# Performance work log

Hardware: AMD Instinct MI355X
Metric: run time of the kernel (lower is better)

## Reference

```python
import jax, jax.numpy as jnp
import numpy as np

B, S, H, K = 4, 2048, 1024, 4
DT, TAU_MIN, TAU_MAX = 0.1, 1.0, 5.0
SCALE = 0.01
LN_EPS = 1e-5


def setup_inputs() -> dict:
    key = jax.random.key(0)
    ks = jax.random.split(key, 8)
    inv = 1.0 / np.sqrt(H)
    return {
        "hidden_states": jax.random.normal(ks[0], (B, S, H), dtype=jnp.float32),
        "conv_w": jax.random.normal(ks[1], (H, K), dtype=jnp.float32) * 0.25,  # depthwise causal conv weights
        "W_rec": jax.random.normal(ks[2], (H, H), dtype=jnp.float32) * inv,    # Linear(H,H,bias=False).weight
        "tau_w1": jax.random.normal(ks[3], (2 * H, H // 2), dtype=jnp.float32) * (1.0 / np.sqrt(2 * H)),
        "tau_b1": jnp.zeros((H // 2,), dtype=jnp.float32),
        "tau_w2": jax.random.normal(ks[4], (H // 2, 1), dtype=jnp.float32) * (1.0 / np.sqrt(H // 2)),
        "tau_b2": jnp.zeros((1,), dtype=jnp.float32),
        "ln_g": jnp.ones((H,), dtype=jnp.float32),
        "ln_b": jnp.zeros((H,), dtype=jnp.float32),
    }


def _shortconv(x, conv_w):
    # depthwise causal conv over seq: x [B,S,H], conv_w [H,K]
    xp = jnp.pad(x, ((0, 0), (K - 1, 0), (0, 0)))
    out = jnp.zeros_like(x)
    for k in range(K):  # K=4, static small loop
        out = out + conv_w[None, None, :, k] * xp[:, k:k + x.shape[1], :]
    return out


def _liquid(x, W_rec, tau_w1, tau_b1, tau_w2, tau_b2, ln_g, ln_b):
    # x: [B,S,H] -> per-step gated recurrence with LayerNorm, via lax.scan
    def step(h, x_t):
        combined = jnp.concatenate([x_t, h], axis=-1)                  # [B,2H]
        tau_raw = jax.nn.sigmoid(
            jnp.tanh(combined @ tau_w1 + tau_b1) @ tau_w2 + tau_b2)    # [B,1]
        tau = TAU_MIN + (TAU_MAX - TAU_MIN) * tau_raw
        f_xh = jnp.tanh(x_t + h @ W_rec.T)                             # [B,H]
        h = h + DT * (-h + f_xh) / tau
        mu = jnp.mean(h, axis=-1, keepdims=True)
        var = jnp.mean((h - mu) ** 2, axis=-1, keepdims=True)
        h = (h - mu) / jnp.sqrt(var + LN_EPS) * ln_g + ln_b            # LayerNorm
        return h, h

    h0 = jnp.zeros((x.shape[0], H), dtype=x.dtype)
    _, liq = jax.lax.scan(step, h0, jnp.swapaxes(x, 0, 1))             # liq [S,B,H]
    return jnp.swapaxes(liq, 0, 1)


def reference(hidden_states, conv_w, W_rec, tau_w1, tau_b1, tau_w2, tau_b2, ln_g, ln_b):
    sc = _shortconv(hidden_states, conv_w)
    liq = _liquid(hidden_states, W_rec, tau_w1, tau_b1, tau_w2, tau_b2, ln_g, ln_b)
    return sc + SCALE * (liq - sc)
```

## Files before the change

### kernel.cpp

```cpp
#include <hip/hip_runtime.h>
#include <math.h>

#define BB   4
#define SS   2048
#define HH   1024
#define HHF  512
#define NWG  192
#define REC_WGS 128
#define NTH  256

__device__ __forceinline__ float dot4f(float4 a, float4 b){
  return a.x*b.x + a.y*b.y + a.z*b.z + a.w*b.w;
}

__device__ __forceinline__ float2 aload2(const float* p){
  unsigned long long v = __hip_atomic_load((const unsigned long long*)p,
                                           __ATOMIC_RELAXED, __HIP_MEMORY_SCOPE_AGENT);
  union { unsigned long long u; float2 f; } c; c.u = v; return c.f;
}
__device__ __forceinline__ void astore1(float* p, float v){
  __hip_atomic_store(p, v, __ATOMIC_RELAXED, __HIP_MEMORY_SCOPE_AGENT);
}
__device__ __forceinline__ float aload1(const float* p){
  return __hip_atomic_load(p, __ATOMIC_RELAXED, __HIP_MEMORY_SCOPE_AGENT);
}

__global__ __launch_bounds__(256) void transpose_w1h(const float* __restrict__ tw1,
                                                     float* __restrict__ w1hT){
  __shared__ float ts[32][33];
  int c  = threadIdx.x & 31;
  int r4 = (threadIdx.x >> 5) * 4;
  int bi = blockIdx.x * 32;
  int bm = blockIdx.y * 32;
  #pragma unroll
  for (int rr = 0; rr < 4; ++rr)
    ts[r4+rr][c] = tw1[(size_t)(1024 + bi + r4 + rr) * 512 + bm + c];
  __syncthreads();
  #pragma unroll
  for (int rr = 0; rr < 4; ++rr)
    w1hT[(size_t)(bm + r4 + rr) * 1024 + bi + c] = ts[c][r4+rr];
}

__global__ __launch_bounds__(256) void gemm_xtau(const float* __restrict__ X,
                                                 const float* __restrict__ tw1,
                                                 const float* __restrict__ b1,
                                                 float* __restrict__ xtau){
  __shared__ float Xs[16][68];
  __shared__ float Ws[16][68];
  const int tid = threadIdx.x;
  const int tx = tid & 15, ty = tid >> 4;
  const int rowbase = blockIdx.y * 64;
  const int colbase = blockIdx.x * 64;
  const int xr  = tid >> 2,  xk4 = (tid & 3) * 4;
  const int wr  = tid >> 4,  wc4 = (tid & 15) * 4;
  float acc[4][4];
  #pragma unroll
  for (int i=0;i<4;++i){
    #pragma unroll
    for (int j=0;j<4;++j) acc[i][j]=0.f;
  }
  for (int k0 = 0; k0 < 1024; k0 += 16){
    float4 xv = *(const float4*)&X  [(size_t)(rowbase + xr)*1024 + k0 + xk4];
    float4 wv = *(const float4*)&tw1[(size_t)(k0 + wr)*512 + colbase + wc4];
    __syncthreads();
    Xs[xk4+0][xr]=xv.x; Xs[xk4+1][xr]=xv.y; Xs[xk4+2][xr]=xv.z; Xs[xk4+3][xr]=xv.w;
    *(float4*)&Ws[wr][wc4] = wv;
    __syncthreads();
    #pragma unroll
    for (int kk=0;kk<16;++kk){
      float4 av = *(const float4*)&Xs[kk][ty*4];
      float4 bv = *(const float4*)&Ws[kk][tx*4];
      acc[0][0]+=av.x*bv.x; acc[0][1]+=av.x*bv.y; acc[0][2]+=av.x*bv.z; acc[0][3]+=av.x*bv.w;
      acc[1][0]+=av.y*bv.x; acc[1][1]+=av.y*bv.y; acc[1][2]+=av.y*bv.z; acc[1][3]+=av.y*bv.w;
      acc[2][0]+=av.z*bv.x; acc[2][1]+=av.z*bv.y; acc[2][2]+=av.z*bv.z; acc[2][3]+=av.z*bv.w;
      acc[3][0]+=av.w*bv.x; acc[3][1]+=av.w*bv.y; acc[3][2]+=av.w*bv.z; acc[3][3]+=av.w*bv.w;
    }
  }
  float4 bias = *(const float4*)&b1[colbase + tx*4];
  #pragma unroll
  for (int i=0;i<4;++i){
    float4 o;
    o.x=acc[i][0]+bias.x; o.y=acc[i][1]+bias.y; o.z=acc[i][2]+bias.z; o.w=acc[i][3]+bias.w;
    *(float4*)&xtau[(size_t)(rowbase + ty*4 + i)*512 + colbase + tx*4] = o;
  }
}

__global__ __launch_bounds__(256, 1) void liquid_kernel(
    const float* __restrict__ X, const float* __restrict__ Wrec,
    const float* __restrict__ w1hT, const float* __restrict__ tw2,
    const float* __restrict__ tb2, const float* __restrict__ lng,
    const float* __restrict__ lnb, const float* __restrict__ xtau,
    float* __restrict__ fbuf, float* __restrict__ tau_slot,
    unsigned int* __restrict__ bar, float* __restrict__ out)
{
  __shared__ float hs[4][1024];
  __shared__ float red_stage[4][8];
  __shared__ float tau_stage[4];
  __shared__ float stat_lds[8];
  __shared__ float w2_lds[8];

  const int tid  = threadIdx.x;
  const int wv   = tid >> 6;
  const int lane = tid & 63;
  const int wg   = blockIdx.x;

  for (int p = tid; p < 4096; p += NTH) (&hs[0][0])[p] = 0.f;

  float4 wreg[2][4];
  #pragma unroll
  for (int rr = 0; rr < 2; ++rr){
    int vrow = wg*8 + wv*2 + rr;
    const float* wrow = (vrow < 1024) ? (Wrec + (size_t)vrow*1024)
                                      : (w1hT + (size_t)(vrow - 1024)*1024);
    #pragma unroll
    for (int k = 0; k < 4; ++k)
      wreg[rr][k] = *(const float4*)&wrow[4*lane + 256*k];
  }
  float4 g4[4], be4[4];
  #pragma unroll
  for (int k = 0; k < 4; ++k){
    g4[k]  = *(const float4*)&lng[4*lane + 256*k];
    be4[k] = *(const float4*)&lnb[4*lane + 256*k];
  }
  const float b2 = tb2[0];
  if (wg >= REC_WGS && tid < 8) w2_lds[tid] = tw2[(wg - REC_WGS)*8 + tid];
  __syncthreads();

  unsigned int target = 0;
  for (int t = 0; t < SS; ++t){
    const int ew = tid >> 3, ea = tid & 7;
    const int erow = (ea >> 2), eb = ea & 3;
    const int elrow = ew*2 + erow;
    float xpre = 0.f;
    if (tid < 32){
      if (wg < REC_WGS)
        xpre = X[((size_t)eb*SS + t)*HH + wg*8 + elrow];
      else
        xpre = xtau[((size_t)eb*SS + t)*HHF + (wg - REC_WGS)*8 + elrow];
    }
    float acc[8];
    #pragma unroll
    for (int a=0;a<8;++a) acc[a]=0.f;
    #pragma unroll
    for (int k=0;k<4;++k){
      const int off = 4*lane + 256*k;
      float4 h0 = *(const float4*)&hs[0][off];
      float4 h1 = *(const float4*)&hs[1][off];
      float4 h2 = *(const float4*)&hs[2][off];
      float4 h3 = *(const float4*)&hs[3][off];
      #pragma unroll
      for (int rr=0;rr<2;++rr){
        acc[rr*4+0] += dot4f(wreg[rr][k], h0);
        acc[rr*4+1] += dot4f(wreg[rr][k], h1);
        acc[rr*4+2] += dot4f(wreg[rr][k], h2);
        acc[rr*4+3] += dot4f(wreg[rr][k], h3);
      }
    }
    #pragma unroll
    for (int a=0;a<8;++a){
      float v = acc[a];
      #pragma unroll
      for (int o=32;o>0;o>>=1) v += __shfl_xor(v, o, 64);
      acc[a]=v;
    }
    if (lane == 0){
      #pragma unroll
      for (int a=0;a<8;++a) red_stage[wv][a] = acc[a];
    }
    __syncthreads();
    if (tid < 32){
      float val = red_stage[ew][ea];
      if (wg < REC_WGS){
        float f = tanhf(xpre + val);
        astore1(&fbuf[(size_t)(t & 1)*4096 + eb*1024 + wg*8 + elrow], f);
      } else {
        float t1 = tanhf(xpre + val);
        float contrib = t1 * w2_lds[elrow];
        contrib += __shfl_xor(contrib, 4, 64);
        contrib += __shfl_xor(contrib, 8, 64);
        contrib += __shfl_xor(contrib, 16, 64);
        if (tid < 4)
          __hip_atomic_fetch_add(&tau_slot[(t % 3)*4 + tid], contrib,
                                 __ATOMIC_RELAXED, __HIP_MEMORY_SCOPE_AGENT);
      }
    }
    __syncthreads();
    asm volatile("" ::: "memory");
    if (tid == 0)
      __hip_atomic_fetch_add(&bar[(wg & 3)*16], 1u, __ATOMIC_RELAXED, __HIP_MEMORY_SCOPE_AGENT);
    target += NWG;
    if (tid == 0){
      int guard = 0;
      while (guard < 200000000){
        unsigned int s = __hip_atomic_load(&bar[0],  __ATOMIC_RELAXED, __HIP_MEMORY_SCOPE_AGENT)
                       + __hip_atomic_load(&bar[16], __ATOMIC_RELAXED, __HIP_MEMORY_SCOPE_AGENT)
                       + __hip_atomic_load(&bar[32], __ATOMIC_RELAXED, __HIP_MEMORY_SCOPE_AGENT)
                       + __hip_atomic_load(&bar[48], __ATOMIC_RELAXED, __HIP_MEMORY_SCOPE_AGENT);
        if (s >= target) break;
        __builtin_amdgcn_s_sleep(1);
        ++guard;
      }
    }
    asm volatile("" ::: "memory");
    __syncthreads();

    float4 f4[4];
    const float* fb = fbuf + (size_t)(t & 1)*4096 + wv*1024;
    #pragma unroll
    for (int k=0;k<4;++k){
      float2 lo = aload2(&fb[4*lane + 256*k]);
      float2 hi = aload2(&fb[4*lane + 256*k + 2]);
      f4[k].x = lo.x; f4[k].y = lo.y; f4[k].z = hi.x; f4[k].w = hi.y;
    }
    if (tid < 4)
      tau_stage[tid] = aload1(&tau_slot[(t % 3)*4 + tid]);
    if (wg == 0 && tid >= 32 && tid < 36)
      astore1(&tau_slot[((t + 2) % 3)*4 + (tid - 32)], 0.f);
    __syncthreads();
    float pre = tau_stage[wv] + b2;
    float sig = 1.f / (1.f + expf(-pre));
    float tau = 1.f + 4.f * sig;
    float al  = 0.1f / tau;
    float s1 = 0.f, s2 = 0.f;
    float4 hp4[4];
    #pragma unroll
    for (int k=0;k<4;++k){
      const int off = 4*lane + 256*k;
      float4 h4 = *(const float4*)&hs[wv][off];
      float4 hp;
      hp.x = h4.x + al*(f4[k].x - h4.x);
      hp.y = h4.y + al*(f4[k].y - h4.y);
      hp.z = h4.z + al*(f4[k].z - h4.z);
      hp.w = h4.w + al*(f4[k].w - h4.w);
      hp4[k] = hp;
      s1 += hp.x + hp.y + hp.z + hp.w;
      s2 += hp.x*hp.x + hp.y*hp.y + hp.z*hp.z + hp.w*hp.w;
    }
    #pragma unroll
    for (int o=32;o>0;o>>=1){
      s1 += __shfl_xor(s1, o, 64);
      s2 += __shfl_xor(s2, o, 64);
    }
    if (lane == 0){ stat_lds[wv*2] = s1; stat_lds[wv*2+1] = s2; }
    __syncthreads();
    float mu   = stat_lds[wv*2]   * (1.f/1024.f);
    float var  = stat_lds[wv*2+1] * (1.f/1024.f) - mu*mu;
    float rstd = rsqrtf(var + 1e-5f);
    #pragma unroll
    for (int k=0;k<4;++k){
      const int off = 4*lane + 256*k;
      float4 hp = hp4[k];
      float4 o4;
      o4.x = (hp.x - mu)*rstd*g4[k].x + be4[k].x;
      o4.y = (hp.y - mu)*rstd*g4[k].y + be4[k].y;
      o4.z = (hp.z - mu)*rstd*g4[k].z + be4[k].z;
      o4.w = (hp.w - mu)*rstd*g4[k].w + be4[k].w;
      *(float4*)&hs[wv][off] = o4;
    }
    __syncthreads();
    if (wg < 16){
      int idx = wg*NTH + tid;
      int ob = idx >> 10, oi = idx & 1023;
      out[((size_t)ob*SS + t)*HH + oi] = hs[ob][oi];
    }
  }
}

__global__ __launch_bounds__(256) void finalize_kernel(const float* __restrict__ X,
                                                       const float* __restrict__ cw,
                                                       float* __restrict__ out){
  size_t gid = (size_t)blockIdx.x * 256 + threadIdx.x;
  size_t gi  = gid * 4;
  int b   = (int)(gi >> 21);
  int rem = (int)(gi & 2097151);
  int t   = rem >> 10;
  int i   = rem & 1023;
  float4 l4 = *(const float4*)&out[gi];
  const float* xb = X + ((size_t)b*SS)*HH + i;
  float4 z4 = make_float4(0.f,0.f,0.f,0.f);
  float4 xk0 = (t >= 3) ? *(const float4*)&xb[(size_t)(t-3)*HH] : z4;
  float4 xk1 = (t >= 2) ? *(const float4*)&xb[(size_t)(t-2)*HH] : z4;
  float4 xk2 = (t >= 1) ? *(const float4*)&xb[(size_t)(t-1)*HH] : z4;
  float4 xk3 =            *(const float4*)&xb[(size_t)t*HH];
  float4 cw0 = *(const float4*)&cw[(i+0)*4];
  float4 cw1 = *(const float4*)&cw[(i+1)*4];
  float4 cw2 = *(const float4*)&cw[(i+2)*4];
  float4 cw3 = *(const float4*)&cw[(i+3)*4];
  float4 sc;
  sc.x = cw0.x*xk0.x + cw0.y*xk1.x + cw0.z*xk2.x + cw0.w*xk3.x;
  sc.y = cw1.x*xk0.y + cw1.y*xk1.y + cw1.z*xk2.y + cw1.w*xk3.y;
  sc.z = cw2.x*xk0.z + cw2.y*xk1.z + cw2.z*xk2.z + cw2.w*xk3.z;
  sc.w = cw3.x*xk0.w + cw3.y*xk1.w + cw3.z*xk2.w + cw3.w*xk3.w;
  float4 o;
  o.x = sc.x + 0.01f*(l4.x - sc.x);
  o.y = sc.y + 0.01f*(l4.y - sc.y);
  o.z = sc.z + 0.01f*(l4.z - sc.z);
  o.w = sc.w + 0.01f*(l4.w - sc.w);
  *(float4*)&out[gi] = o;
}

extern "C" void kernel_launch(void* const* d_in, const int* in_sizes, int n_in,
                              void* d_out, int out_size, void* d_ws, size_t ws_size,
                              hipStream_t stream) {
  const float* X     = (const float*)d_in[0];
  const float* convw = (const float*)d_in[1];
  const float* Wrec  = (const float*)d_in[2];
  const float* tw1   = (const float*)d_in[3];
  const float* tb1   = (const float*)d_in[4];
  const float* tw2   = (const float*)d_in[5];
  const float* tb2   = (const float*)d_in[6];
  const float* lng   = (const float*)d_in[7];
  const float* lnb   = (const float*)d_in[8];
  float* out = (float*)d_out;
  float* wsf = (float*)d_ws;

  unsigned int* bar = (unsigned int*)d_ws;
  float* tau_slot = wsf + 64;
  float* fbuf     = wsf + 128;
  float* w1hT     = wsf + 8448;
  float* xtau     = w1hT + 512*1024;

  hipMemsetAsync(d_ws, 0, 512, stream);
  transpose_w1h<<<dim3(32,16), dim3(256), 0, stream>>>(tw1, w1hT);
  gemm_xtau   <<<dim3(8,128),  dim3(256), 0, stream>>>(X, tw1, tb1, xtau);
  liquid_kernel<<<dim3(NWG),   dim3(NTH), 0, stream>>>(X, Wrec, w1hT, tw2, tb2,
                                                       lng, lnb, xtau, fbuf,
                                                       tau_slot, bar, out);
  finalize_kernel<<<dim3(8192), dim3(256), 0, stream>>>(X, convw, out);
}
```

Measured before the change: 9.829 ms.

## Replace global counter barrier with per-value step-tagged flag polling

Removes the atomic counter grid barrier and the tau atomic accumulation. Each produced value is tagged with a per-step offset (2*(t+1) for f, 8*(t+1) for tau partials), so consumers poll the data itself until every element carries the current step's tag. This removes the barrier round trip, several __syncthreads and the LDS staging, and double-buffers the hidden state in LDS. The risks are precision loss from adding large offsets to small values as t grows, and correctness that depends on the value-range tolerance checks.

After: 19.23 ms (median of 4 runs). 1.96x slower.

```diff
diff --git a/kernel.cpp b/kernel.cpp
--- a/kernel.cpp
+++ b/kernel.cpp
@@ -1,7 +1,6 @@
 #include <hip/hip_runtime.h>
 #include <math.h>
 
-#define BB   4
 #define SS   2048
 #define HH   1024
 #define HHF  512
@@ -90,21 +89,17 @@
     const float* __restrict__ w1hT, const float* __restrict__ tw2,
     const float* __restrict__ tb2, const float* __restrict__ lng,
     const float* __restrict__ lnb, const float* __restrict__ xtau,
-    float* __restrict__ fbuf, float* __restrict__ tau_slot,
-    unsigned int* __restrict__ bar, float* __restrict__ out)
+    float* __restrict__ fbuf, float* __restrict__ taup,
+    float* __restrict__ out)
 {
-  __shared__ float hs[4][1024];
-  __shared__ float red_stage[4][8];
-  __shared__ float tau_stage[4];
-  __shared__ float stat_lds[8];
-  __shared__ float w2_lds[8];
+  __shared__ float hs[2][4][1024];
 
   const int tid  = threadIdx.x;
   const int wv   = tid >> 6;
   const int lane = tid & 63;
   const int wg   = blockIdx.x;
 
-  for (int p = tid; p < 4096; p += NTH) (&hs[0][0])[p] = 0.f;
+  for (int p = tid; p < 8192; p += NTH) (&hs[0][0][0])[p] = 0.f;
 
   float4 wreg[2][4];
   #pragma unroll
@@ -123,31 +118,37 @@
     be4[k] = *(const float4*)&lnb[4*lane + 256*k];
   }
   const float b2 = tb2[0];
-  if (wg >= REC_WGS && tid < 8) w2_lds[tid] = tw2[(wg - REC_WGS)*8 + tid];
+  float w2r0 = 0.f, w2r1 = 0.f;
+  if (wg >= REC_WGS){
+    w2r0 = tw2[(wg - REC_WGS)*8 + wv*2 + 0];
+    w2r1 = tw2[(wg - REC_WGS)*8 + wv*2 + 1];
+  }
   __syncthreads();
 
-  unsigned int target = 0;
   for (int t = 0; t < SS; ++t){
-    const int ew = tid >> 3, ea = tid & 7;
-    const int erow = (ea >> 2), eb = ea & 3;
-    const int elrow = ew*2 + erow;
+    const int cur = t & 1, nxt = cur ^ 1;
+    const float fbase = 2.f*(float)(t+1);
+    const float tbase = 8.f*(float)(t+1);
+
     float xpre = 0.f;
-    if (tid < 32){
+    if (lane < 8){
+      const int rr = lane >> 2, b = lane & 3;
       if (wg < REC_WGS)
-        xpre = X[((size_t)eb*SS + t)*HH + wg*8 + elrow];
+        xpre = X[((size_t)b*SS + t)*HH + wg*8 + wv*2 + rr];
       else
-        xpre = xtau[((size_t)eb*SS + t)*HHF + (wg - REC_WGS)*8 + elrow];
-    }
+        xpre = xtau[((size_t)b*SS + t)*HHF + (wg - REC_WGS)*8 + wv*2 + rr];
+    }
+
     float acc[8];
     #pragma unroll
     for (int a=0;a<8;++a) acc[a]=0.f;
     #pragma unroll
     for (int k=0;k<4;++k){
       const int off = 4*lane + 256*k;
-      float4 h0 = *(const float4*)&hs[0][off];
-      float4 h1 = *(const float4*)&hs[1][off];
-      float4 h2 = *(const float4*)&hs[2][off];
-      float4 h3 = *(const float4*)&hs[3][off];
+      float4 h0 = *(const float4*)&hs[cur][0][off];
+      float4 h1 = *(const float4*)&hs[cur][1][off];
+      float4 h2 = *(const float4*)&hs[cur][2][off];
+      float4 h3 = *(const float4*)&hs[cur][3][off];
       #pragma unroll
       for (int rr=0;rr<2;++rr){
         acc[rr*4+0] += dot4f(wreg[rr][k], h0);
@@ -163,75 +164,70 @@
       for (int o=32;o>0;o>>=1) v += __shfl_xor(v, o, 64);
       acc[a]=v;
     }
-    if (lane == 0){
+    float sel = acc[0];
+    sel = (lane==1)?acc[1]:sel; sel = (lane==2)?acc[2]:sel;
+    sel = (lane==3)?acc[3]:sel; sel = (lane==4)?acc[4]:sel;
+    sel = (lane==5)?acc[5]:sel; sel = (lane==6)?acc[6]:sel;
+    sel = (lane==7)?acc[7]:sel;
+    float fval = tanhf(xpre + sel);
+
+    if (wg < REC_WGS){
+      if (lane < 8)
+        astore1(&fbuf[cur*4096 + (lane&3)*1024 + wg*8 + wv*2 + (lane>>2)],
+                fbase + fval);
+    } else {
+      float w2s = (lane & 4) ? w2r1 : w2r0;
+      float contrib = fval * w2s;
+      contrib += __shfl_xor(contrib, 4, 64);
+      if (lane < 4)
+        astore1(&taup[cur*1024 + lane*256 + (wg - REC_WGS)*4 + wv],
+                tbase + contrib);
+    }
+
+    const float* fb = fbuf + cur*4096 + wv*1024;
+    float2 pr[8]; float tv[4];
+    #pragma unroll
+    for (int q=0;q<8;++q)
+      pr[q] = aload2(&fb[(q>>1)*256 + 4*lane + (q&1)*2]);
+    #pragma unroll
+    for (int j=0;j<4;++j)
+      tv[j] = aload1(&taup[cur*1024 + wv*256 + lane + 64*j]);
+    int guard = 0;
+    while (true){
+      bool all = true;
       #pragma unroll
-      for (int a=0;a<8;++a) red_stage[wv][a] = acc[a];
-    }
-    __syncthreads();
-    if (tid < 32){
-      float val = red_stage[ew][ea];
-      if (wg < REC_WGS){
-        float f = tanhf(xpre + val);
-        astore1(&fbuf[(size_t)(t & 1)*4096 + eb*1024 + wg*8 + elrow], f);
-      } else {
-        float t1 = tanhf(xpre + val);
-        float contrib = t1 * w2_lds[elrow];
-        contrib += __shfl_xor(contrib, 4, 64);
-        contrib += __shfl_xor(contrib, 8, 64);
-        contrib += __shfl_xor(contrib, 16, 64);
-        if (tid < 4)
-          __hip_atomic_fetch_add(&tau_slot[(t % 3)*4 + tid], contrib,
-                                 __ATOMIC_RELAXED, __HIP_MEMORY_SCOPE_AGENT);
+      for (int q=0;q<8;++q){
+        bool ok = (fabsf(pr[q].x - fbase) < 1.5f) && (fabsf(pr[q].y - fbase) < 1.5f);
+        if (!ok){ all = false; pr[q] = aload2(&fb[(q>>1)*256 + 4*lane + (q&1)*2]); }
       }
-    }
-    __syncthreads();
-    asm volatile("" ::: "memory");
-    if (tid == 0)
-      __hip_atomic_fetch_add(&bar[(wg & 3)*16], 1u, __ATOMIC_RELAXED, __HIP_MEMORY_SCOPE_AGENT);
-    target += NWG;
-    if (tid == 0){
-      int guard = 0;
-      while (guard < 200000000){
-        unsigned int s = __hip_atomic_load(&bar[0],  __ATOMIC_RELAXED, __HIP_MEMORY_SCOPE_AGENT)
-                       + __hip_atomic_load(&bar[16], __ATOMIC_RELAXED, __HIP_MEMORY_SCOPE_AGENT)
-                       + __hip_atomic_load(&bar[32], __ATOMIC_RELAXED, __HIP_MEMORY_SCOPE_AGENT)
-                       + __hip_atomic_load(&bar[48], __ATOMIC_RELAXED, __HIP_MEMORY_SCOPE_AGENT);
-        if (s >= target) break;
-        __builtin_amdgcn_s_sleep(1);
-        ++guard;
+      #pragma unroll
+      for (int j=0;j<4;++j){
+        if (!(fabsf(tv[j] - tbase) < 4.f)){
+          all = false; tv[j] = aload1(&taup[cur*1024 + wv*256 + lane + 64*j]);
+        }
       }
-    }
-    asm volatile("" ::: "memory");
-    __syncthreads();
-
-    float4 f4[4];
-    const float* fb = fbuf + (size_t)(t & 1)*4096 + wv*1024;
-    #pragma unroll
-    for (int k=0;k<4;++k){
-      float2 lo = aload2(&fb[4*lane + 256*k]);
-      float2 hi = aload2(&fb[4*lane + 256*k + 2]);
-      f4[k].x = lo.x; f4[k].y = lo.y; f4[k].z = hi.x; f4[k].w = hi.y;
-    }
-    if (tid < 4)
-      tau_stage[tid] = aload1(&tau_slot[(t % 3)*4 + tid]);
-    if (wg == 0 && tid >= 32 && tid < 36)
-      astore1(&tau_slot[((t + 2) % 3)*4 + (tid - 32)], 0.f);
-    __syncthreads();
-    float pre = tau_stage[wv] + b2;
+      if (all) break;
+      if (++guard > 100000) break;
+    }
+
+    float tpart = (tv[0]-tbase)+(tv[1]-tbase)+(tv[2]-tbase)+(tv[3]-tbase);
+    #pragma unroll
+    for (int o=32;o>0;o>>=1) tpart += __shfl_xor(tpart, o, 64);
+    float pre = tpart + b2;
     float sig = 1.f / (1.f + expf(-pre));
-    float tau = 1.f + 4.f * sig;
-    float al  = 0.1f / tau;
+    float al  = 0.1f / (1.f + 4.f*sig);
+
     float s1 = 0.f, s2 = 0.f;
     float4 hp4[4];
     #pragma unroll
     for (int k=0;k<4;++k){
       const int off = 4*lane + 256*k;
-      float4 h4 = *(const float4*)&hs[wv][off];
+      float4 h4 = *(const float4*)&hs[cur][wv][off];
       float4 hp;
-      hp.x = h4.x + al*(f4[k].x - h4.x);
-      hp.y = h4.y + al*(f4[k].y - h4.y);
-      hp.z = h4.z + al*(f4[k].z - h4.z);
-      hp.w = h4.w + al*(f4[k].w - h4.w);
+      hp.x = h4.x + al*((pr[2*k  ].x - fbase) - h4.x);
+      hp.y = h4.y + al*((pr[2*k  ].y - fbase) - h4.y);
+      hp.z = h4.z + al*((pr[2*k+1].x - fbase) - h4.z);
+      hp.w = h4.w + al*((pr[2*k+1].y - fbase) - h4.w);
       hp4[k] = hp;
       s1 += hp.x + hp.y + hp.z + hp.w;
       s2 += hp.x*hp.x + hp.y*hp.y + hp.z*hp.z + hp.w*hp.w;
@@ -241,10 +237,8 @@
       s1 += __shfl_xor(s1, o, 64);
       s2 += __shfl_xor(s2, o, 64);
     }
-    if (lane == 0){ stat_lds[wv*2] = s1; stat_lds[wv*2+1] = s2; }
-    __syncthreads();
-    float mu   = stat_lds[wv*2]   * (1.f/1024.f);
-    float var  = stat_lds[wv*2+1] * (1.f/1024.f) - mu*mu;
+    float mu   = s1 * (1.f/1024.f);
+    float var  = s2 * (1.f/1024.f) - mu*mu;
     float rstd = rsqrtf(var + 1e-5f);
     #pragma unroll
     for (int k=0;k<4;++k){
@@ -255,14 +249,14 @@
       o4.y = (hp.y - mu)*rstd*g4[k].y + be4[k].y;
       o4.z = (hp.z - mu)*rstd*g4[k].z + be4[k].z;
       o4.w = (hp.w - mu)*rstd*g4[k].w + be4[k].w;
-      *(float4*)&hs[wv][off] = o4;
-    }
-    __syncthreads();
-    if (wg < 16){
-      int idx = wg*NTH + tid;
-      int ob = idx >> 10, oi = idx & 1023;
-      out[((size_t)ob*SS + t)*HH + oi] = hs[ob][oi];
-    }
+      *(float4*)&hs[nxt][wv][off] = o4;
+      if (wg < 16 && (wg >> 2) == k && (lane >> 4) == (wg & 3))
+        *(float4*)&out[((size_t)wv*SS + t)*HH + off] = o4;
+    }
+
+    asm volatile("s_waitcnt lgkmcnt(0)" ::: "memory");
+    __builtin_amdgcn_sched_barrier(0);
+    __builtin_amdgcn_s_barrier();
   }
 }
 
@@ -314,17 +308,16 @@
   float* out = (float*)d_out;
   float* wsf = (float*)d_ws;
 
-  unsigned int* bar = (unsigned int*)d_ws;
-  float* tau_slot = wsf + 64;
-  float* fbuf     = wsf + 128;
-  float* w1hT     = wsf + 8448;
-  float* xtau     = w1hT + 512*1024;
-
-  hipMemsetAsync(d_ws, 0, 512, stream);
+  float* fbuf = wsf;
+  float* taup = wsf + 8192;
+  float* w1hT = wsf + 10240;
+  float* xtau = w1hT + 512*1024;
+
+  hipMemsetAsync(d_ws, 0, 40960, stream);
   transpose_w1h<<<dim3(32,16), dim3(256), 0, stream>>>(tw1, w1hT);
   gemm_xtau   <<<dim3(8,128),  dim3(256), 0, stream>>>(X, tw1, tb1, xtau);
   liquid_kernel<<<dim3(NWG),   dim3(NTH), 0, stream>>>(X, Wrec, w1hT, tw2, tb2,
                                                        lng, lnb, xtau, fbuf,
-                                                       tau_slot, bar, out);
+                                                       taup, out);
   finalize_kernel<<<dim3(8192), dim3(256), 0, stream>>>(X, convw, out);
 }
```
